# Performance work log

Measured on AMD Instinct MI355X. Metric: run time of the kernel, lower is better.

The kernel has to match this reference:

```python
import jax, jax.numpy as jnp
import numpy as np

N_EMBED = 1024
N_HEAD = 16
HEAD_DIM = N_EMBED // N_HEAD
B, T = 64, 256
EPS = 1e-5


def _layernorm(x, w, b):
    mu = jnp.mean(x, axis=-1, keepdims=True)
    var = jnp.mean(jnp.square(x - mu), axis=-1, keepdims=True)
    return (x - mu) * jax.lax.rsqrt(var + EPS) * w + b


def setup_inputs() -> dict:
    key = jax.random.key(0)
    ks = jax.random.split(key, 8)
    s = lambda fan_in: 1.0 / np.sqrt(fan_in)
    return {
        "x": jax.random.normal(ks[0], (B, T, N_EMBED), dtype=jnp.float32),
        "ln1_w": jnp.ones((N_EMBED,), jnp.float32),
        "ln1_b": jnp.zeros((N_EMBED,), jnp.float32),
        # weights stored [in, out] (transposed vs torch Linear)
        "w_attn": jax.random.normal(ks[1], (N_EMBED, 3 * N_EMBED), jnp.float32) * s(N_EMBED),
        "b_attn": jnp.zeros((3 * N_EMBED,), jnp.float32),
        "w_proj": jax.random.normal(ks[2], (N_EMBED, N_EMBED), jnp.float32) * s(N_EMBED),
        "b_proj": jnp.zeros((N_EMBED,), jnp.float32),
        "ln2_w": jnp.ones((N_EMBED,), jnp.float32),
        "ln2_b": jnp.zeros((N_EMBED,), jnp.float32),
        "w_fc": jax.random.normal(ks[3], (N_EMBED, 4 * N_EMBED), jnp.float32) * s(N_EMBED),
        "b_fc": jnp.zeros((4 * N_EMBED,), jnp.float32),
        "w_out": jax.random.normal(ks[4], (4 * N_EMBED, N_EMBED), jnp.float32) * s(4 * N_EMBED),
        "b_out": jnp.zeros((N_EMBED,), jnp.float32),
    }


def reference(x, ln1_w, ln1_b, w_attn, b_attn, w_proj, b_proj,
              ln2_w, ln2_b, w_fc, b_fc, w_out, b_out):
    Bs, Ts, C = x.shape
    # --- attention branch (pre-norm) ---
    h = _layernorm(x, ln1_w, ln1_b)
    qkv = h @ w_attn + b_attn                      # [B,T,3C]
    q, k, v = jnp.split(qkv, 3, axis=-1)
    q = q.reshape(Bs, Ts, N_HEAD, HEAD_DIM).transpose(0, 2, 1, 3)  # [B,H,T,D]
    k = k.reshape(Bs, Ts, N_HEAD, HEAD_DIM).transpose(0, 2, 1, 3)
    v = v.reshape(Bs, Ts, N_HEAD, HEAD_DIM).transpose(0, 2, 1, 3)
    att = jnp.einsum("bhqd,bhkd->bhqk", q, k) * (1.0 / np.sqrt(HEAD_DIM))
    causal = jnp.tril(jnp.ones((Ts, Ts), dtype=bool))
    att = jnp.where(causal, att, -jnp.inf)
    att = jax.nn.softmax(att, axis=-1)
    y = jnp.einsum("bhqk,bhkd->bhqd", att, v)      # [B,H,T,D]
    y = y.transpose(0, 2, 1, 3).reshape(Bs, Ts, C)
    x = x + (y @ w_proj + b_proj)
    # --- MLP branch (pre-norm) ---
    h = _layernorm(x, ln2_w, ln2_b)
    h = jax.nn.gelu(h @ w_fc + b_fc, approximate=False)
    x = x + (h @ w_out + b_out)
    return x
```

## Files before the change

kernel.cpp:

```cpp
#include <hip/hip_runtime.h>
#include <math.h>


#define C_DIM   1024
#define NHEAD   16
#define HDIM    64
#define TSEQ    256
#define BATCH   64

typedef __attribute__((ext_vector_type(4))) float fx4;
typedef __attribute__((ext_vector_type(8))) short sx8;

typedef const __attribute__((address_space(1))) void* gvp;
typedef __attribute__((address_space(3))) void* lvp;

__device__ __forceinline__ void gload16(const ushort* g, ushort* l) {
    __builtin_amdgcn_global_load_lds((gvp)g, (lvp)l, 16, 0, 0);
}

__device__ __forceinline__ ushort f2bf(float f) {
    uint x = __float_as_uint(f);
    x += 0x7fffu + ((x >> 16) & 1u);
    return (ushort)(x >> 16);
}
__device__ __forceinline__ float bf2f(ushort u) {
    return __uint_as_float(((uint)u) << 16);
}

__global__ __launch_bounds__(256)
void wconv(const float* __restrict__ W, ushort* __restrict__ Wt, int K, int N)
{
    __shared__ float T[64][65];
    const int kt = blockIdx.x << 6, nt = blockIdx.y << 6;
    const int ln = threadIdx.x & 63, g4 = threadIdx.x >> 6;
    #pragma unroll
    for (int i = 0; i < 16; ++i) {
        const int r = i * 4 + g4;
        T[r][ln] = W[(size_t)(kt + r) * N + nt + ln];
    }
    __syncthreads();
    #pragma unroll
    for (int i = 0; i < 16; ++i) {
        const int r = i * 4 + g4;
        Wt[(size_t)(nt + r) * K + kt + ln] = f2bf(T[ln][r]);
    }
}

__global__ __launch_bounds__(256)
void ln_bf16(const float* __restrict__ x, const float* __restrict__ w,
             const float* __restrict__ b, ushort* __restrict__ out)
{
    const int row = blockIdx.x;
    const int tid = threadIdx.x;
    const float4 v = reinterpret_cast<const float4*>(x + (size_t)row * C_DIM)[tid];

    float s  = v.x + v.y + v.z + v.w;
    float ss = v.x * v.x + v.y * v.y + v.z * v.z + v.w * v.w;
    #pragma unroll
    for (int off = 32; off > 0; off >>= 1) {
        s  += __shfl_down(s, off);
        ss += __shfl_down(ss, off);
    }
    __shared__ float rs[4], rss[4];
    const int wid = tid >> 6, lane = tid & 63;
    if (lane == 0) { rs[wid] = s; rss[wid] = ss; }
    __syncthreads();
    if (tid == 0) {
        const float S  = rs[0] + rs[1] + rs[2] + rs[3];
        const float SS = rss[0] + rss[1] + rss[2] + rss[3];
        const float mu  = S * (1.0f / C_DIM);
        const float var = SS * (1.0f / C_DIM) - mu * mu;
        rs[0]  = mu;
        rss[0] = rsqrtf(var + 1e-5f);
    }
    __syncthreads();
    const float mu = rs[0], rstd = rss[0];

    const float4 wv = reinterpret_cast<const float4*>(w)[tid];
    const float4 bv = reinterpret_cast<const float4*>(b)[tid];
    ushort4 o;
    o.x = f2bf((v.x - mu) * rstd * wv.x + bv.x);
    o.y = f2bf((v.y - mu) * rstd * wv.y + bv.y);
    o.z = f2bf((v.z - mu) * rstd * wv.z + bv.z);
    o.w = f2bf((v.w - mu) * rstd * wv.w + bv.w);
    reinterpret_cast<ushort4*>(out + (size_t)row * C_DIM)[tid] = o;
}

template<int EPI>
__global__ __launch_bounds__(256)
void gemm_mfma(const ushort* __restrict__ A, const ushort* __restrict__ Wt,
               const float* __restrict__ bias, const float* __restrict__ res,
               void* __restrict__ outv, int M, int N, int K)
{
    __shared__ ushort As[128 * 32];
    __shared__ ushort Bs[128 * 32];

    const int tid  = threadIdx.x;
    const int lane = tid & 63;
    const int wid  = tid >> 6;
    const int wr   = (wid >> 1) << 6;
    const int wc   = (wid & 1) << 6;
    const int bm = blockIdx.x << 7;
    const int bn = blockIdx.y << 7;

    const int srow = tid >> 2;
    const int spos = tid & 3;
    const int skg  = spos ^ ((srow >> 1) & 3);
    const ushort* pa0 = A  + (size_t)(bm + srow)      * K + skg * 8;
    const ushort* pa1 = A  + (size_t)(bm + srow + 64) * K + skg * 8;
    const ushort* pb0 = Wt + (size_t)(bn + srow)      * K + skg * 8;
    const ushort* pb1 = Wt + (size_t)(bn + srow + 64) * K + skg * 8;
    ushort* lA0 = As + wid * 512;
    ushort* lA1 = As + wid * 512 + 2048;
    ushort* lB0 = Bs + wid * 512;
    ushort* lB1 = Bs + wid * 512 + 2048;

    const int frow = lane & 15;
    const int fpos = ((lane >> 4) ^ ((frow >> 1) & 3)) * 8;
    int aoff[4], boff[4];
    #pragma unroll
    for (int i = 0; i < 4; ++i) {
        aoff[i] = (wr + i * 16 + frow) * 32 + fpos;
        boff[i] = (wc + i * 16 + frow) * 32 + fpos;
    }

    fx4 acc[4][4] = {};
    const int nk = K >> 5;

    for (int t = 0; t < nk; ++t) {
        const int ko = t << 5;
        __syncthreads();
        gload16(pa0 + ko, lA0);
        gload16(pa1 + ko, lA1);
        gload16(pb0 + ko, lB0);
        gload16(pb1 + ko, lB1);
        __syncthreads();

        sx8 af[4], bf[4];
        #pragma unroll
        for (int i = 0; i < 4; ++i) af[i] = *(const sx8*)&As[aoff[i]];
        #pragma unroll
        for (int i = 0; i < 4; ++i) bf[i] = *(const sx8*)&Bs[boff[i]];
        #pragma unroll
        for (int i = 0; i < 4; ++i)
            #pragma unroll
            for (int j = 0; j < 4; ++j)
                acc[i][j] = __builtin_amdgcn_mfma_f32_16x16x32_bf16(
                    af[i], bf[j], acc[i][j], 0, 0, 0);
    }

    const int r0 = bm + wr + (lane >> 4) * 4;
    const int c0 = bn + wc + (lane & 15);
    #pragma unroll
    for (int i = 0; i < 4; ++i) {
        #pragma unroll
        for (int r = 0; r < 4; ++r) {
            const int row = r0 + i * 16 + r;
            #pragma unroll
            for (int j = 0; j < 4; ++j) {
                const int col = c0 + j * 16;
                float v = acc[i][j][r] + bias[col];
                if (EPI == 1) {
                    v += res[(size_t)row * N + col];
                    ((float*)outv)[(size_t)row * N + col] = v;
                } else if (EPI == 2) {
                    v = 0.5f * v * (1.0f + erff(v * 0.70710678118654752f));
                    ((ushort*)outv)[(size_t)row * N + col] = f2bf(v);
                } else {
                    ((ushort*)outv)[(size_t)row * N + col] = f2bf(v);
                }
            }
        }
    }
}

__global__ __launch_bounds__(256, 1)
void attn_mfma(const ushort* __restrict__ qkv, ushort* __restrict__ y)
{
    __shared__ ushort Ks[256 * 72];
    __shared__ ushort Vt[64 * 264];
    __shared__ ushort Pl[4][64 * 72];

    const int bl = blockIdx.x >> 4;
    const int h  = blockIdx.x & 15;
    const size_t base = (size_t)bl * TSEQ * 3072 + (size_t)h * HDIM;

    const int tid  = threadIdx.x;
    const int lane = tid & 63;
    const int w    = tid >> 6;
    const int c15  = lane & 15;
    const int grp  = lane >> 4;

    {
        const int kv = tid;
        const ushort* kp = qkv + base + (size_t)kv * 3072 + 1024;
        const ushort* vp = qkv + base + (size_t)kv * 3072 + 2048;
        #pragma unroll
        for (int j = 0; j < 8; ++j) {
            sx8 k8 = *(const sx8*)(kp + j * 8);
            *(sx8*)&Ks[kv * 72 + j * 8] = k8;
            sx8 v8 = *(const sx8*)(vp + j * 8);
            #pragma unroll
            for (int e = 0; e < 8; ++e)
                Vt[(j * 8 + e) * 264 + kv] = (ushort)v8[e];
        }
    }

    sx8 aq[4][2];
    #pragma unroll
    for (int m = 0; m < 4; ++m)
        #pragma unroll
        for (int kc = 0; kc < 2; ++kc) {
            const int qr = w * 64 + m * 16 + c15;
            aq[m][kc] = *(const sx8*)(qkv + base + (size_t)qr * 3072 + kc * 32 + grp * 8);
        }

    __syncthreads();

    fx4 oacc[4][4] = {};
    float m_s[4][4], l_s[4][4];
    #pragma unroll
    for (int m = 0; m < 4; ++m)
        #pragma unroll
        for (int r = 0; r < 4; ++r) { m_s[m][r] = -INFINITY; l_s[m][r] = 0.0f; }

    for (int t = 0; t <= w; ++t) {
        const int kt = t * 64;
        const bool diag = (t == w);

        fx4 s[4][4] = {};
        #pragma unroll
        for (int kc = 0; kc < 2; ++kc)
            #pragma unroll
            for (int n = 0; n < 4; ++n) {
                sx8 bk = *(const sx8*)&Ks[(kt + n * 16 + c15) * 72 + kc * 32 + grp * 8];
                #pragma unroll
                for (int m = 0; m < 4; ++m)
                    s[m][n] = __builtin_amdgcn_mfma_f32_16x16x32_bf16(
                        aq[m][kc], bk, s[m][n], 0, 0, 0);
            }

        #pragma unroll
        for (int m = 0; m < 4; ++m)
            #pragma unroll
            for (int n = 0; n < 4; ++n)
                #pragma unroll
                for (int r = 0; r < 4; ++r) {
                    float v = s[m][n][r] * 0.125f;
                    if (diag && (n * 16 + c15) > (m * 16 + grp * 4 + r)) v = -1e30f;
                    s[m][n][r] = v;
                }

        #pragma unroll
        for (int m = 0; m < 4; ++m)
            #pragma unroll
            for (int r = 0; r < 4; ++r) {
                float mx = fmaxf(fmaxf(s[m][0][r], s[m][1][r]),
                                 fmaxf(s[m][2][r], s[m][3][r]));
                #pragma unroll
                for (int off = 1; off < 16; off <<= 1)
                    mx = fmaxf(mx, __shfl_xor(mx, off));
                const float mnew = fmaxf(m_s[m][r], mx);
                const float cold = __expf(m_s[m][r] - mnew);
                m_s[m][r] = mnew;
                float rsum = 0.0f;
                #pragma unroll
                for (int n = 0; n < 4; ++n) {
                    const float p = __expf(s[m][n][r] - mnew);
                    s[m][n][r] = p;
                    rsum += p;
                }
                #pragma unroll
                for (int off = 1; off < 16; off <<= 1)
                    rsum += __shfl_xor(rsum, off);
                l_s[m][r] = l_s[m][r] * cold + rsum;
                #pragma unroll
                for (int dn = 0; dn < 4; ++dn)
                    oacc[m][dn][r] *= cold;
            }

        #pragma unroll
        for (int m = 0; m < 4; ++m)
            #pragma unroll
            for (int n = 0; n < 4; ++n)
                #pragma unroll
                for (int r = 0; r < 4; ++r)
                    Pl[w][(m * 16 + grp * 4 + r) * 72 + n * 16 + c15] =
                        f2bf(s[m][n][r]);

        #pragma unroll
        for (int kc = 0; kc < 2; ++kc) {
            sx8 ap[4];
            #pragma unroll
            for (int m = 0; m < 4; ++m)
                ap[m] = *(const sx8*)&Pl[w][(m * 16 + c15) * 72 + kc * 32 + grp * 8];
            #pragma unroll
            for (int dn = 0; dn < 4; ++dn) {
                sx8 bv = *(const sx8*)&Vt[(dn * 16 + c15) * 264 + kt + kc * 32 + grp * 8];
                #pragma unroll
                for (int m = 0; m < 4; ++m)
                    oacc[m][dn] = __builtin_amdgcn_mfma_f32_16x16x32_bf16(
                        ap[m], bv, oacc[m][dn], 0, 0, 0);
            }
        }
    }

    #pragma unroll
    for (int m = 0; m < 4; ++m)
        #pragma unroll
        for (int r = 0; r < 4; ++r) {
            const float inv = 1.0f / l_s[m][r];
            const int row = bl * TSEQ + w * 64 + m * 16 + grp * 4 + r;
            ushort* yp = y + (size_t)row * C_DIM + h * HDIM;
            #pragma unroll
            for (int dn = 0; dn < 4; ++dn)
                yp[dn * 16 + c15] = f2bf(oacc[m][dn][r] * inv);
        }
}

extern "C" void kernel_launch(void* const* d_in, const int* in_sizes, int n_in,
                              void* d_out, int out_size, void* d_ws, size_t ws_size,
                              hipStream_t stream)
{
    const float* x      = (const float*)d_in[0];
    const float* ln1_w  = (const float*)d_in[1];
    const float* ln1_b  = (const float*)d_in[2];
    const float* w_attn = (const float*)d_in[3];
    const float* b_attn = (const float*)d_in[4];
    const float* w_proj = (const float*)d_in[5];
    const float* b_proj = (const float*)d_in[6];
    const float* ln2_w  = (const float*)d_in[7];
    const float* ln2_b  = (const float*)d_in[8];
    const float* w_fc   = (const float*)d_in[9];
    const float* b_fc   = (const float*)d_in[10];
    const float* w_out  = (const float*)d_in[11];
    const float* b_out  = (const float*)d_in[12];
    float* out = (float*)d_out;

    ushort* wbf     = (ushort*)d_ws;
    ushort* wt_attn = wbf;
    ushort* wt_proj = wbf + 3145728;
    ushort* wt_fc   = wbf + 4194304;
    ushort* wt_out  = wbf + 8388608;
    const size_t wbytes = 12582912ull * 2;

    int nchunk = 64;
    for (int cand = 1; cand <= 64; cand *= 2) {
        const size_t rows = (size_t)(BATCH / cand) * TSEQ;
        if (wbytes + rows * 10240ull <= ws_size) { nchunk = cand; break; }
    }
    const int bchunk = BATCH / nchunk;
    const int rows   = bchunk * TSEQ;

    ushort* hbuf = wbf + 12582912;
    ushort* qkvb = hbuf + (size_t)rows * 1024;
    ushort* ybuf = qkvb + (size_t)rows * 3072;
    ushort* act  = qkvb;

    wconv<<<dim3(16, 48), 256, 0, stream>>>(w_attn, wt_attn, 1024, 3072);
    wconv<<<dim3(16, 16), 256, 0, stream>>>(w_proj, wt_proj, 1024, 1024);
    wconv<<<dim3(16, 64), 256, 0, stream>>>(w_fc,   wt_fc,   1024, 4096);
    wconv<<<dim3(64, 16), 256, 0, stream>>>(w_out,  wt_out,  4096, 1024);

    for (int c = 0; c < nchunk; ++c) {
        const size_t r0 = (size_t)c * rows;
        const float* xc = x   + r0 * C_DIM;
        float*       oc = out + r0 * C_DIM;
        ln_bf16<<<rows, 256, 0, stream>>>(xc, ln1_w, ln1_b, hbuf);
        gemm_mfma<0><<<dim3(rows / 128, 3072 / 128), 256, 0, stream>>>(
            hbuf, wt_attn, b_attn, nullptr, qkvb, rows, 3072, 1024);
        attn_mfma<<<bchunk * NHEAD, 256, 0, stream>>>(qkvb, ybuf);
        gemm_mfma<1><<<dim3(rows / 128, 1024 / 128), 256, 0, stream>>>(
            ybuf, wt_proj, b_proj, xc, oc, rows, 1024, 1024);
    }

    for (int c = 0; c < nchunk; ++c) {
        const size_t r0 = (size_t)c * rows;
        float* oc = out + r0 * C_DIM;
        ln_bf16<<<rows, 256, 0, stream>>>(oc, ln2_w, ln2_b, hbuf);
        gemm_mfma<2><<<dim3(rows / 128, 4096 / 128), 256, 0, stream>>>(
            hbuf, wt_fc, b_fc, nullptr, act, rows, 4096, 1024);
        gemm_mfma<1><<<dim3(rows / 128, 1024 / 128), 256, 0, stream>>>(
            act, wt_out, b_out, oc, oc, rows, 1024, 4096);
    }
}
```

Measured before the change: 1.019 ms.

## Double-buffer LDS tiles in the bf16 MFMA GEMM to overlap loads with compute

Splits the GEMM's shared-memory A and B tiles into two buffers. The next K-slice is issued with global_load_lds while MFMAs run on the current slice, and the loop uses one barrier per iteration instead of two. The aim is to hide global memory latency behind matrix math. This doubles LDS use per block, which may lower occupancy. The compiler's vmcnt waits around the async LDS loads may also serialize the overlap in practice.

Measured after the change: 976.0 us. 1.04x faster.

```diff
diff --git a/kernel.cpp b/kernel.cpp
--- a/kernel.cpp
+++ b/kernel.cpp
@@ -92,8 +92,8 @@
                const float* __restrict__ bias, const float* __restrict__ res,
                void* __restrict__ outv, int M, int N, int K)
 {
-    __shared__ ushort As[128 * 32];
-    __shared__ ushort Bs[128 * 32];
+    __shared__ ushort As[2][128 * 32];
+    __shared__ ushort Bs[2][128 * 32];
 
     const int tid  = threadIdx.x;
     const int lane = tid & 63;
@@ -110,10 +110,7 @@
     const ushort* pa1 = A  + (size_t)(bm + srow + 64) * K + skg * 8;
     const ushort* pb0 = Wt + (size_t)(bn + srow)      * K + skg * 8;
     const ushort* pb1 = Wt + (size_t)(bn + srow + 64) * K + skg * 8;
-    ushort* lA0 = As + wid * 512;
-    ushort* lA1 = As + wid * 512 + 2048;
-    ushort* lB0 = Bs + wid * 512;
-    ushort* lB1 = Bs + wid * 512 + 2048;
+    const int wo = wid * 512;
 
     const int frow = lane & 15;
     const int fpos = ((lane >> 4) ^ ((frow >> 1) & 3)) * 8;
@@ -127,26 +124,36 @@
     fx4 acc[4][4] = {};
     const int nk = K >> 5;
 
+    gload16(pa0, &As[0][wo]);
+    gload16(pa1, &As[0][wo + 2048]);
+    gload16(pb0, &Bs[0][wo]);
+    gload16(pb1, &Bs[0][wo + 2048]);
+    __syncthreads();
+
     for (int t = 0; t < nk; ++t) {
-        const int ko = t << 5;
-        __syncthreads();
-        gload16(pa0 + ko, lA0);
-        gload16(pa1 + ko, lA1);
-        gload16(pb0 + ko, lB0);
-        gload16(pb1 + ko, lB1);
-        __syncthreads();
+        const int cur = t & 1;
+        if (t + 1 < nk) {
+            const int nb = cur ^ 1;
+            const int ko = (t + 1) << 5;
+            gload16(pa0 + ko, &As[nb][wo]);
+            gload16(pa1 + ko, &As[nb][wo + 2048]);
+            gload16(pb0 + ko, &Bs[nb][wo]);
+            gload16(pb1 + ko, &Bs[nb][wo + 2048]);
+        }
 
         sx8 af[4], bf[4];
         #pragma unroll
-        for (int i = 0; i < 4; ++i) af[i] = *(const sx8*)&As[aoff[i]];
-        #pragma unroll
-        for (int i = 0; i < 4; ++i) bf[i] = *(const sx8*)&Bs[boff[i]];
+        for (int i = 0; i < 4; ++i) af[i] = *(const sx8*)&As[cur][aoff[i]];
+        #pragma unroll
+        for (int i = 0; i < 4; ++i) bf[i] = *(const sx8*)&Bs[cur][boff[i]];
         #pragma unroll
         for (int i = 0; i < 4; ++i)
             #pragma unroll
             for (int j = 0; j < 4; ++j)
                 acc[i][j] = __builtin_amdgcn_mfma_f32_16x16x32_bf16(
                     af[i], bf[j], acc[i][j], 0, 0, 0);
+
+        __syncthreads();
     }
 
     const int r0 = bm + wr + (lane >> 4) * 4;
```
